# Kernel optimization log

Measured on AMD Instinct MI355X. Metric: run time of the kernel, lower is better.

The kernel has to match this reference:

```python
import jax, jax.numpy as jnp
import numpy as np

EPS = 0.0  # init eps

def setup_inputs() -> dict:
    key = jax.random.key(0)
    k1, k2, k3 = jax.random.split(key, 3)
    n_nodes = 100000
    n_edges = 6400000
    edge_weight = jax.random.uniform(k1, (n_edges,), dtype=jnp.float32)  # non-negative, required by norm='both'
    src = jax.random.randint(k2, (n_edges,), 0, n_nodes, dtype=jnp.int32)
    dst = jax.random.randint(k3, (n_edges,), 0, n_nodes, dtype=jnp.int32)
    return {"edge_weight": edge_weight, "src": src, "dst": dst, "num_nodes": n_nodes}

def reference(edge_weight, src, dst, num_nodes):
    # norm='both': out-degree (weighted) per source node via reversed graph,
    # in-degree (weighted) per destination node; both as segment sums over edges.
    out_deg = jax.ops.segment_sum(edge_weight, src, num_segments=num_nodes) + EPS
    in_deg = jax.ops.segment_sum(edge_weight, dst, num_segments=num_nodes) + EPS
    src_norm = out_deg ** -0.5  # [N]
    dst_norm = in_deg ** -0.5   # [N]
    # gather per-edge norms and multiply with edge weight
    return src_norm[src] * dst_norm[dst] * edge_weight
```

## Files before the change

### kernel.cpp

```cpp
#include <hip/hip_runtime.h>
#include <hip/hip_fp16.h>


#define N_NODES 100000
#define TWO_N   (2 * N_NODES)
#define THREADS 1024
#define GBLK    1024
#define KMAX    7
#define SCALE_F   512.0f
#define INV_SCALE 0.001953125f

__global__ __launch_bounds__(THREADS, 4)
void hist_kernel(const float4* __restrict__ w4,
                 const int4* __restrict__ src4,
                 const int4* __restrict__ dst4,
                 const float* __restrict__ w,
                 const int* __restrict__ src,
                 const int* __restrict__ dst,
                 unsigned* __restrict__ parts,
                 int n4, int n_edges, int P, int C, int bins, int chunk4,
                 int swz)
{
    extern __shared__ unsigned lds[];
    int j, c;
    if (swz) {
        const int x = blockIdx.x & 7;
        const int r = blockIdx.x >> 3;
        j = r % P;
        c = x + 8 * (r / P);
    } else {
        j = blockIdx.x / C;
        c = blockIdx.x - j * C;
    }
    const int lo = j * bins;

    for (int k = threadIdx.x; k < bins; k += THREADS) lds[k] = 0;
    __syncthreads();

    const int beg = c * chunk4;
    const int end = min(n4, beg + chunk4);
    const int t   = threadIdx.x;

#define QUAD(wv, sv, dv)                                                      \
    do {                                                                      \
        unsigned v0 = (unsigned)((wv).x * SCALE_F + 0.5f);                    \
        unsigned v1 = (unsigned)((wv).y * SCALE_F + 0.5f);                    \
        unsigned v2 = (unsigned)((wv).z * SCALE_F + 0.5f);                    \
        unsigned v3 = (unsigned)((wv).w * SCALE_F + 0.5f);                    \
        int a0 = (sv).x - lo, a1 = (sv).y - lo, a2 = (sv).z - lo, a3 = (sv).w - lo; \
        int b0 = (dv).x - lo, b1 = (dv).y - lo, b2 = (dv).z - lo, b3 = (dv).w - lo; \
        if ((unsigned)a0 < (unsigned)bins) atomicAdd(&lds[a0], v0);           \
        if ((unsigned)a1 < (unsigned)bins) atomicAdd(&lds[a1], v1);           \
        if ((unsigned)a2 < (unsigned)bins) atomicAdd(&lds[a2], v2);           \
        if ((unsigned)a3 < (unsigned)bins) atomicAdd(&lds[a3], v3);           \
        if ((unsigned)b0 < (unsigned)bins) atomicAdd(&lds[b0], v0 << 16);     \
        if ((unsigned)b1 < (unsigned)bins) atomicAdd(&lds[b1], v1 << 16);     \
        if ((unsigned)b2 < (unsigned)bins) atomicAdd(&lds[b2], v2 << 16);     \
        if ((unsigned)b3 < (unsigned)bins) atomicAdd(&lds[b3], v3 << 16);     \
    } while (0)

    {
        const int total = end - beg;
        const int trips = (total + 2 * THREADS - 1) / (2 * THREADS);
        int i = beg + t;

        float4 wc0, wc1, wn0, wn1;
        int4   sc0, sc1, sn0, sn1, dc0, dc1, dn0, dn1;
        bool   pc0, pc1, pn0, pn1;

        pn0 = i < end;
        pn1 = (i + THREADS) < end;
        if (pn0) { wn0 = w4[i];           sn0 = src4[i];           dn0 = dst4[i]; }
        if (pn1) { wn1 = w4[i + THREADS]; sn1 = src4[i + THREADS]; dn1 = dst4[i + THREADS]; }

        for (int tr = 0; tr < trips; ++tr) {
            wc0 = wn0; sc0 = sn0; dc0 = dn0; pc0 = pn0;
            wc1 = wn1; sc1 = sn1; dc1 = dn1; pc1 = pn1;

            const int ni = i + 2 * THREADS;
            pn0 = (tr + 1 < trips) && (ni < end);
            pn1 = (tr + 1 < trips) && ((ni + THREADS) < end);
            if (pn0) { wn0 = w4[ni];           sn0 = src4[ni];           dn0 = dst4[ni]; }
            if (pn1) { wn1 = w4[ni + THREADS]; sn1 = src4[ni + THREADS]; dn1 = dst4[ni + THREADS]; }

            __builtin_amdgcn_sched_barrier(0);

            if (pc0) QUAD(wc0, sc0, dc0);
            if (pc1) QUAD(wc1, sc1, dc1);
            i = ni;
        }
    }
#undef QUAD

    if (c == C - 1 && threadIdx.x == 0) {
        for (int e = n4 * 4; e < n_edges; ++e) {
            unsigned v = (unsigned)(w[e] * SCALE_F + 0.5f);
            int a = src[e] - lo;
            int b = dst[e] - lo;
            if ((unsigned)a < (unsigned)bins) atomicAdd(&lds[a], v);
            if ((unsigned)b < (unsigned)bins) atomicAdd(&lds[b], v << 16);
        }
    }

    __syncthreads();
    unsigned* op = parts + ((size_t)j * C + c) * bins;
    for (int k = threadIdx.x; k < bins; k += THREADS)
        __builtin_nontemporal_store(lds[k], op + k);
}

__global__ void reduce_rsqrt_kernel(const unsigned* __restrict__ parts,
                                    __half* __restrict__ normh,
                                    int P, int C, int bins)
{
    int i = blockIdx.x * blockDim.x + threadIdx.x;
    if (i >= N_NODES) return;
    int p = i / bins;
    int b = i - p * bins;
    const unsigned* base = parts + ((size_t)p * C) * bins + b;
    unsigned lo0 = 0, hi0 = 0, lo1 = 0, hi1 = 0, lo2 = 0, hi2 = 0, lo3 = 0, hi3 = 0;
    int c = 0;
    for (; c + 3 < C; c += 4) {
        unsigned v0 = base[(size_t)(c + 0) * bins];
        unsigned v1 = base[(size_t)(c + 1) * bins];
        unsigned v2 = base[(size_t)(c + 2) * bins];
        unsigned v3 = base[(size_t)(c + 3) * bins];
        lo0 += v0 & 0xFFFFu; hi0 += v0 >> 16;
        lo1 += v1 & 0xFFFFu; hi1 += v1 >> 16;
        lo2 += v2 & 0xFFFFu; hi2 += v2 >> 16;
        lo3 += v3 & 0xFFFFu; hi3 += v3 >> 16;
    }
    for (; c < C; ++c) {
        unsigned v = base[(size_t)c * bins];
        lo0 += v & 0xFFFFu; hi0 += v >> 16;
    }
    unsigned lo_s = lo0 + lo1 + lo2 + lo3;
    unsigned hi_s = hi0 + hi1 + hi2 + hi3;
    normh[i]           = __float2half(1.0f / sqrtf((float)lo_s * INV_SCALE));
    normh[N_NODES + i] = __float2half(1.0f / sqrtf((float)hi_s * INV_SCALE));
}

__global__ void degree_atomic_kernel(const float* __restrict__ w,
                                     const int* __restrict__ src,
                                     const int* __restrict__ dst,
                                     float* __restrict__ deg,
                                     int n_edges)
{
    int i = blockIdx.x * blockDim.x + threadIdx.x;
    int stride = gridDim.x * blockDim.x;
    for (; i < n_edges; i += stride) {
        float wi = w[i];
        atomicAdd(&deg[src[i]], wi);
        atomicAdd(&deg[N_NODES + dst[i]], wi);
    }
}

__global__ void rsqrt_half_kernel(const float* __restrict__ deg,
                                  __half* __restrict__ normh, int n)
{
    int i = blockIdx.x * blockDim.x + threadIdx.x;
    if (i < n) normh[i] = __float2half(1.0f / sqrtf(deg[i]));
}

__global__ __launch_bounds__(GBLK)
void prod_kernel(const float4* __restrict__ w4,
                 const int4* __restrict__ src4,
                 const int4* __restrict__ dst4,
                 const __half* __restrict__ srcn_h,
                 const __half* __restrict__ dstn_h,
                 float4* __restrict__ out4,
                 int n4, int n_edges, int qpb, int binsh,
                 const float* __restrict__ w,
                 const int* __restrict__ src,
                 const int* __restrict__ dst,
                 float* __restrict__ out)
{
    extern __shared__ __half lh[];
    const int q0   = blockIdx.x * qpb;
    const int qend = min(n4, q0 + qpb);
    const int t    = threadIdx.x;

    float4 pr[KMAX];
    int4   sv[KMAX], dv[KMAX];
    bool   val[KMAX];

#pragma unroll
    for (int k = 0; k < KMAX; ++k) {
        const int q = q0 + k * GBLK + t;
        val[k] = q < qend;
        if (val[k]) {
            pr[k] = w4[q];
            sv[k] = src4[q];
            dv[k] = dst4[q];
        }
    }

    for (int phase = 0; phase < 2; ++phase) {
        const __half* tab = phase ? dstn_h : srcn_h;
        for (int lo = 0; lo < N_NODES; lo += binsh) {
            const int len = min(binsh, N_NODES - lo);
            const int len8 = len >> 3;
            const uint4* tsrc = (const uint4*)(tab + lo);
            uint4* ldst = (uint4*)lh;
            for (int k2 = t; k2 < len8; k2 += GBLK) ldst[k2] = tsrc[k2];
            for (int k2 = (len8 << 3) + t; k2 < len; k2 += GBLK) lh[k2] = tab[lo + k2];
            __syncthreads();

#pragma unroll
            for (int k = 0; k < KMAX; ++k) {
                if (!val[k]) continue;
                const int4 iv = phase ? dv[k] : sv[k];
                unsigned a;
                a = (unsigned)(iv.x - lo); if (a < (unsigned)len) pr[k].x *= __half2float(lh[a]);
                a = (unsigned)(iv.y - lo); if (a < (unsigned)len) pr[k].y *= __half2float(lh[a]);
                a = (unsigned)(iv.z - lo); if (a < (unsigned)len) pr[k].z *= __half2float(lh[a]);
                a = (unsigned)(iv.w - lo); if (a < (unsigned)len) pr[k].w *= __half2float(lh[a]);
            }
            __syncthreads();
        }
    }

#pragma unroll
    for (int k = 0; k < KMAX; ++k) {
        const int q = q0 + k * GBLK + t;
        if (val[k]) out4[q] = pr[k];
    }

    if (blockIdx.x == 0 && t == 0) {
        for (int e = n4 * 4; e < n_edges; ++e)
            out[e] = __half2float(srcn_h[src[e]]) * __half2float(dstn_h[dst[e]]) * w[e];
    }
}

extern "C" void kernel_launch(void* const* d_in, const int* in_sizes, int n_in,
                              void* d_out, int out_size, void* d_ws, size_t ws_size,
                              hipStream_t stream)
{
    const float* w   = (const float*)d_in[0];
    const int*   src = (const int*)d_in[1];
    const int*   dst = (const int*)d_in[2];
    const int E  = in_sizes[0];
    const int n4 = E >> 2;
    float* out = (float*)d_out;

    __half* normh = (__half*)d_ws;
    char* scratch = (char*)d_ws + (1 << 20);
    unsigned* parts = (unsigned*)scratch;
    float* degf = (float*)scratch;
    size_t avail_u = (ws_size > (1u << 20)) ? (ws_size - (1 << 20)) / 4 : 0;

    const int cands[3] = {163840, 131072, 81920};
    int lds_hist = 65536;
    for (int tC = 0; tC < 3; ++tC)
        if (hipFuncSetAttribute((const void*)hist_kernel,
                                hipFuncAttributeMaxDynamicSharedMemorySize,
                                cands[tC]) == hipSuccess) { lds_hist = cands[tC]; break; }
    int lds_prod = 65536;
    for (int tC = 0; tC < 3; ++tC)
        if (hipFuncSetAttribute((const void*)prod_kernel,
                                hipFuncAttributeMaxDynamicSharedMemorySize,
                                cands[tC]) == hipSuccess) { lds_prod = cands[tC]; break; }

    const int bins = lds_hist / 4;
    const int P = (N_NODES + bins - 1) / bins;

    const int blk_per_cu = 163840 / lds_hist;
    int C = (256 * blk_per_cu) / P;
    const size_t per_chunk_u = (size_t)P * (size_t)bins;
    if (avail_u < per_chunk_u) C = 0;
    else {
        int cmax = (int)(avail_u / per_chunk_u);
        if (C > cmax) C = cmax;
    }

    int swz = 0;
    if (C >= 8) { C &= ~7; swz = 1; }

    if (C >= 1) {
        const int chunk4 = (n4 + C - 1) / C;
        hist_kernel<<<P * C, THREADS, (size_t)lds_hist, stream>>>(
            (const float4*)w, (const int4*)src, (const int4*)dst,
            w, src, dst, parts, n4, E, P, C, bins, chunk4, swz);
        reduce_rsqrt_kernel<<<(N_NODES + 255) / 256, 256, 0, stream>>>(
            parts, normh, P, C, bins);
    } else {
        hipMemsetAsync(degf, 0, (size_t)TWO_N * sizeof(float), stream);
        degree_atomic_kernel<<<2048, 256, 0, stream>>>(w, src, dst, degf, E);
        rsqrt_half_kernel<<<(TWO_N + 255) / 256, 256, 0, stream>>>(degf, normh, TWO_N);
    }

    {
        const int binsh = lds_prod / 2;
        const int maxq = KMAX * GBLK;
        int C2 = (n4 + maxq - 1) / maxq;
        if (C2 < 256) C2 = 256;
        const int qpb = (n4 + C2 - 1) / C2;
        prod_kernel<<<C2, GBLK, (size_t)lds_prod, stream>>>(
            (const float4*)w, (const int4*)src, (const int4*)dst,
            normh, normh + N_NODES, (float4*)out,
            n4, E, qpb, binsh, w, src, dst, out);
    }
}
```

Baseline: 72.26 us.

## Double-buffer norm table staging in LDS, merging src and dst passes

The product kernel now stages matching ranges of the src and dst norm tables together in each pass, instead of running two separate phases. It double-buffers LDS so the global loads for the next range are issued into registers while the current range is used. This is meant to hide global-to-LDS staging latency and halve the number of sync rounds. In exchange each buffer holds a quarter of the LDS, so there are more passes, and the launch bound now requests 4 waves per EU, which may pressure registers.

```diff
diff --git a/kernel.cpp b/kernel.cpp
--- a/kernel.cpp
+++ b/kernel.cpp
@@ -7,6 +7,7 @@
 #define THREADS 1024
 #define GBLK    1024
 #define KMAX    7
+#define FMAX    5
 #define SCALE_F   512.0f
 #define INV_SCALE 0.001953125f
 
@@ -161,14 +162,14 @@
     if (i < n) normh[i] = __float2half(1.0f / sqrtf(deg[i]));
 }
 
-__global__ __launch_bounds__(GBLK)
+__global__ __launch_bounds__(GBLK, 4)
 void prod_kernel(const float4* __restrict__ w4,
                  const int4* __restrict__ src4,
                  const int4* __restrict__ dst4,
                  const __half* __restrict__ srcn_h,
                  const __half* __restrict__ dstn_h,
                  float4* __restrict__ out4,
-                 int n4, int n_edges, int qpb, int binsh,
+                 int n4, int n_edges, int qpb, int NR,
                  const float* __restrict__ w,
                  const int* __restrict__ src,
                  const int* __restrict__ dst,
@@ -178,11 +179,13 @@
     const int q0   = blockIdx.x * qpb;
     const int qend = min(n4, q0 + qpb);
     const int t    = threadIdx.x;
+    const int passes  = (N_NODES + NR - 1) / NR;
+    const int half_u4 = NR >> 3;
+    const int tot_u4  = NR >> 2;
 
     float4 pr[KMAX];
     int4   sv[KMAX], dv[KMAX];
     bool   val[KMAX];
-
 #pragma unroll
     for (int k = 0; k < KMAX; ++k) {
         const int q = q0 + k * GBLK + t;
@@ -194,30 +197,67 @@
         }
     }
 
-    for (int phase = 0; phase < 2; ++phase) {
-        const __half* tab = phase ? dstn_h : srcn_h;
-        for (int lo = 0; lo < N_NODES; lo += binsh) {
-            const int len = min(binsh, N_NODES - lo);
-            const int len8 = len >> 3;
-            const uint4* tsrc = (const uint4*)(tab + lo);
-            uint4* ldst = (uint4*)lh;
-            for (int k2 = t; k2 < len8; k2 += GBLK) ldst[k2] = tsrc[k2];
-            for (int k2 = (len8 << 3) + t; k2 < len; k2 += GBLK) lh[k2] = tab[lo + k2];
+    uint4 fr[FMAX];
+
+#define STAGE_LOAD(p)                                                         \
+    do {                                                                      \
+        const int base_ = (p) * NR;                                           \
+        const uint4* gs_ = (const uint4*)(srcn_h + base_);                    \
+        const uint4* gd_ = (const uint4*)(dstn_h + base_);                    \
+        _Pragma("unroll")                                                     \
+        for (int k_ = 0; k_ < FMAX; ++k_) {                                   \
+            const int idx_ = t + k_ * GBLK;                                   \
+            if (idx_ < tot_u4)                                                \
+                fr[k_] = (idx_ < half_u4) ? gs_[idx_] : gd_[idx_ - half_u4];  \
+        }                                                                     \
+    } while (0)
+
+#define STAGE_WRITE(b)                                                        \
+    do {                                                                      \
+        uint4* lb_ = (uint4*)(lh + (size_t)(b) * 2 * NR);                     \
+        _Pragma("unroll")                                                     \
+        for (int k_ = 0; k_ < FMAX; ++k_) {                                   \
+            const int idx_ = t + k_ * GBLK;                                   \
+            if (idx_ < tot_u4) lb_[idx_] = fr[k_];                            \
+        }                                                                     \
+    } while (0)
+
+    STAGE_LOAD(0);
+    STAGE_WRITE(0);
+    __syncthreads();
+
+    int buf = 0;
+    for (int p = 0; p < passes; ++p) {
+        const bool more = (p + 1 < passes);
+        if (more) STAGE_LOAD(p + 1);
+        __builtin_amdgcn_sched_barrier(0);
+
+        const int lo = p * NR;
+        const unsigned lenU = (unsigned)min(NR, N_NODES - lo);
+        const __half* ls  = lh + (size_t)buf * 2 * NR;
+        const __half* ldt = ls + NR;
+#pragma unroll
+        for (int k = 0; k < KMAX; ++k) {
+            if (!val[k]) continue;
+            unsigned a;
+            a = (unsigned)(sv[k].x - lo); if (a < lenU) pr[k].x *= __half2float(ls[a]);
+            a = (unsigned)(sv[k].y - lo); if (a < lenU) pr[k].y *= __half2float(ls[a]);
+            a = (unsigned)(sv[k].z - lo); if (a < lenU) pr[k].z *= __half2float(ls[a]);
+            a = (unsigned)(sv[k].w - lo); if (a < lenU) pr[k].w *= __half2float(ls[a]);
+            a = (unsigned)(dv[k].x - lo); if (a < lenU) pr[k].x *= __half2float(ldt[a]);
+            a = (unsigned)(dv[k].y - lo); if (a < lenU) pr[k].y *= __half2float(ldt[a]);
+            a = (unsigned)(dv[k].z - lo); if (a < lenU) pr[k].z *= __half2float(ldt[a]);
+            a = (unsigned)(dv[k].w - lo); if (a < lenU) pr[k].w *= __half2float(ldt[a]);
+        }
+        __syncthreads();
+        if (more) {
+            STAGE_WRITE(buf ^ 1);
             __syncthreads();
-
-#pragma unroll
-            for (int k = 0; k < KMAX; ++k) {
-                if (!val[k]) continue;
-                const int4 iv = phase ? dv[k] : sv[k];
-                unsigned a;
-                a = (unsigned)(iv.x - lo); if (a < (unsigned)len) pr[k].x *= __half2float(lh[a]);
-                a = (unsigned)(iv.y - lo); if (a < (unsigned)len) pr[k].y *= __half2float(lh[a]);
-                a = (unsigned)(iv.z - lo); if (a < (unsigned)len) pr[k].z *= __half2float(lh[a]);
-                a = (unsigned)(iv.w - lo); if (a < (unsigned)len) pr[k].w *= __half2float(lh[a]);
-            }
-            __syncthreads();
-        }
-    }
+            buf ^= 1;
+        }
+    }
+#undef STAGE_LOAD
+#undef STAGE_WRITE
 
 #pragma unroll
     for (int k = 0; k < KMAX; ++k) {
@@ -289,7 +329,7 @@
     }
 
     {
-        const int binsh = lds_prod / 2;
+        const int NR = lds_prod / 8;
         const int maxq = KMAX * GBLK;
         int C2 = (n4 + maxq - 1) / maxq;
         if (C2 < 256) C2 = 256;
@@ -297,6 +337,6 @@
         prod_kernel<<<C2, GBLK, (size_t)lds_prod, stream>>>(
             (const float4*)w, (const int4*)src, (const int4*)dst,
             normh, normh + N_NODES, (float4*)out,
-            n4, E, qpb, binsh, w, src, dst, out);
-    }
-}
+            n4, E, qpb, NR, w, src, dst, out);
+    }
+}
```

Result: slower. 96.11 us (+33.0%).

## Merge src/dst norm passes in prod kernel and raise occupancy with smaller LDS tiles

Applied to the files above, without the earlier changes.

The product kernel used to sweep the source-norm table and then the destination-norm table as two separate phases. It now stages matching slices of both tables into LDS in each pass and applies both multiplies in one loop. LDS per block is cut to 80 KB, edges per thread drop from 7 to 4, a minimum-occupancy launch bound is added, and the grid rises to at least 512 blocks. The goal is two resident blocks per CU, so more loads are in flight and LDS fills overlap with compute. The cost is more passes per block and more total table-staging traffic from L2 across the larger grid.

```diff
diff --git a/kernel.cpp b/kernel.cpp
--- a/kernel.cpp
+++ b/kernel.cpp
@@ -6,7 +6,7 @@
 #define TWO_N   (2 * N_NODES)
 #define THREADS 1024
 #define GBLK    1024
-#define KMAX    7
+#define KMAX    4
 #define SCALE_F   512.0f
 #define INV_SCALE 0.001953125f
 
@@ -161,14 +161,14 @@
     if (i < n) normh[i] = __float2half(1.0f / sqrtf(deg[i]));
 }
 
-__global__ __launch_bounds__(GBLK)
+__global__ __launch_bounds__(GBLK, 8)
 void prod_kernel(const float4* __restrict__ w4,
                  const int4* __restrict__ src4,
                  const int4* __restrict__ dst4,
                  const __half* __restrict__ srcn_h,
                  const __half* __restrict__ dstn_h,
                  float4* __restrict__ out4,
-                 int n4, int n_edges, int qpb, int binsh,
+                 int n4, int n_edges, int qpb, int NR,
                  const float* __restrict__ w,
                  const int* __restrict__ src,
                  const int* __restrict__ dst,
@@ -178,11 +178,13 @@
     const int q0   = blockIdx.x * qpb;
     const int qend = min(n4, q0 + qpb);
     const int t    = threadIdx.x;
+    const int passes  = (N_NODES + NR - 1) / NR;
+    const int half_u4 = NR >> 3;
+    const int tot_u4  = NR >> 2;
 
     float4 pr[KMAX];
     int4   sv[KMAX], dv[KMAX];
     bool   val[KMAX];
-
 #pragma unroll
     for (int k = 0; k < KMAX; ++k) {
         const int q = q0 + k * GBLK + t;
@@ -194,28 +196,34 @@
         }
     }
 
-    for (int phase = 0; phase < 2; ++phase) {
-        const __half* tab = phase ? dstn_h : srcn_h;
-        for (int lo = 0; lo < N_NODES; lo += binsh) {
-            const int len = min(binsh, N_NODES - lo);
-            const int len8 = len >> 3;
-            const uint4* tsrc = (const uint4*)(tab + lo);
-            uint4* ldst = (uint4*)lh;
-            for (int k2 = t; k2 < len8; k2 += GBLK) ldst[k2] = tsrc[k2];
-            for (int k2 = (len8 << 3) + t; k2 < len; k2 += GBLK) lh[k2] = tab[lo + k2];
-            __syncthreads();
-
+    for (int p = 0; p < passes; ++p) {
+        if (p > 0) __syncthreads();
+        {
+            const int base_ = p * NR;
+            const uint4* gs = (const uint4*)(srcn_h + base_);
+            const uint4* gd = (const uint4*)(dstn_h + base_);
+            uint4* lb = (uint4*)lh;
+            for (int idx = t; idx < tot_u4; idx += GBLK)
+                lb[idx] = (idx < half_u4) ? gs[idx] : gd[idx - half_u4];
+        }
+        __syncthreads();
+
+        const int lo = p * NR;
+        const unsigned lenU = (unsigned)min(NR, N_NODES - lo);
+        const __half* ls  = lh;
+        const __half* ldt = lh + NR;
 #pragma unroll
-            for (int k = 0; k < KMAX; ++k) {
-                if (!val[k]) continue;
-                const int4 iv = phase ? dv[k] : sv[k];
-                unsigned a;
-                a = (unsigned)(iv.x - lo); if (a < (unsigned)len) pr[k].x *= __half2float(lh[a]);
-                a = (unsigned)(iv.y - lo); if (a < (unsigned)len) pr[k].y *= __half2float(lh[a]);
-                a = (unsigned)(iv.z - lo); if (a < (unsigned)len) pr[k].z *= __half2float(lh[a]);
-                a = (unsigned)(iv.w - lo); if (a < (unsigned)len) pr[k].w *= __half2float(lh[a]);
-            }
-            __syncthreads();
+        for (int k = 0; k < KMAX; ++k) {
+            if (!val[k]) continue;
+            unsigned a;
+            a = (unsigned)(sv[k].x - lo); if (a < lenU) pr[k].x *= __half2float(ls[a]);
+            a = (unsigned)(sv[k].y - lo); if (a < lenU) pr[k].y *= __half2float(ls[a]);
+            a = (unsigned)(sv[k].z - lo); if (a < lenU) pr[k].z *= __half2float(ls[a]);
+            a = (unsigned)(sv[k].w - lo); if (a < lenU) pr[k].w *= __half2float(ls[a]);
+            a = (unsigned)(dv[k].x - lo); if (a < lenU) pr[k].x *= __half2float(ldt[a]);
+            a = (unsigned)(dv[k].y - lo); if (a < lenU) pr[k].y *= __half2float(ldt[a]);
+            a = (unsigned)(dv[k].z - lo); if (a < lenU) pr[k].z *= __half2float(ldt[a]);
+            a = (unsigned)(dv[k].w - lo); if (a < lenU) pr[k].w *= __half2float(ldt[a]);
         }
     }
 
@@ -255,10 +263,10 @@
                                 hipFuncAttributeMaxDynamicSharedMemorySize,
                                 cands[tC]) == hipSuccess) { lds_hist = cands[tC]; break; }
     int lds_prod = 65536;
-    for (int tC = 0; tC < 3; ++tC)
-        if (hipFuncSetAttribute((const void*)prod_kernel,
-                                hipFuncAttributeMaxDynamicSharedMemorySize,
-                                cands[tC]) == hipSuccess) { lds_prod = cands[tC]; break; }
+    if (hipFuncSetAttribute((const void*)prod_kernel,
+                            hipFuncAttributeMaxDynamicSharedMemorySize,
+                            81920) == hipSuccess)
+        lds_prod = 81920;
 
     const int bins = lds_hist / 4;
     const int P = (N_NODES + bins - 1) / bins;
@@ -289,14 +297,14 @@
     }
 
     {
-        const int binsh = lds_prod / 2;
+        const int NR = lds_prod / 4;
         const int maxq = KMAX * GBLK;
         int C2 = (n4 + maxq - 1) / maxq;
-        if (C2 < 256) C2 = 256;
+        if (C2 < 512) C2 = 512;
         const int qpb = (n4 + C2 - 1) / C2;
         prod_kernel<<<C2, GBLK, (size_t)lds_prod, stream>>>(
             (const float4*)w, (const int4*)src, (const int4*)dst,
             normh, normh + N_NODES, (float4*)out,
-            n4, E, qpb, binsh, w, src, dst, out);
-    }
-}
+            n4, E, qpb, NR, w, src, dst, out);
+    }
+}
```

Result: faster. 68.76 us (-4.8%).
